# Kernel tuning notes

Hardware: AMD Instinct MI355X
Metric: run time of the kernel (lower is better)

The kernel has to match this reference:

```python
import jax, jax.numpy as jnp
import numpy as np

B, S, D, V = 2, 2048, 1024, 50257
GAMMA = 1.0
IGNORE = -100


def setup_inputs() -> dict:
    key = jax.random.key(0)
    k1, k2, k3, k4 = jax.random.split(key, 4)
    embeddings = jax.random.normal(k1, (B, S, D), dtype=jnp.float32)
    W = jax.random.normal(k2, (V, D), dtype=jnp.float32) * (D ** -0.5)
    b = jnp.zeros((V,), dtype=jnp.float32)
    labels = jax.random.randint(k3, (B, S), 0, V, dtype=jnp.int64)
    input_ids = jax.random.randint(k4, (B, S), 0, V, dtype=jnp.int64)
    return {"embeddings": embeddings, "W": W, "b": b, "labels": labels, "input_ids": input_ids}


def _focal_loss(embeddings, W, b, labels):
    # logits: [B, S, V]
    logits = jnp.einsum('bsd,vd->bsv', embeddings, W) + b
    shift_logits = logits[:, :-1, :].reshape(-1, V)          # [N, V]
    shift_labels = labels[:, 1:].reshape(-1)                  # [N]
    valid = shift_labels != IGNORE
    safe = jnp.where(valid, shift_labels, 0)
    logp = jax.nn.log_softmax(shift_logits, axis=-1)
    ce = -jnp.take_along_axis(logp, safe[:, None], axis=-1)[:, 0]
    ce = jnp.where(valid, ce, 0.0)                            # ignore_index -> 0 loss
    pt = jax.lax.stop_gradient(jnp.exp(-ce))
    w = (1.0 - pt) ** GAMMA
    alpha = 1.0 / jnp.mean(w)
    loss = alpha * w * ce
    return jnp.mean(loss)


def reference(embeddings, W, b, labels, input_ids):
    return _focal_loss(embeddings, W, b, labels)
```

## Files before the change

### kernel.cpp

```cpp
#include <hip/hip_runtime.h>
#include <hip/hip_bf16.h>
#include <cstdint>

#define SDIM   2048
#define DDIM   1024
#define VDIM   50257
#define VPAD   50304
#define NROWS  4094
#define MPAD   4096
#define NTM    32
#define NTN    393
#define NCHUNK (NTN * 2)
#define IGNORE_IDX (-100)

typedef __bf16 bf16x8 __attribute__((ext_vector_type(8)));
typedef float  f32x4  __attribute__((ext_vector_type(4)));

__device__ static inline unsigned short f2bf(float f) {
    union { float f; uint32_t u; } v; v.f = f;
    uint32_t u = v.u;
    return (unsigned short)((u + 0x7FFFu + ((u >> 16) & 1u)) >> 16);
}

__device__ static inline void gload_lds16(const void* g, void* l) {
    __builtin_amdgcn_global_load_lds(
        (const __attribute__((address_space(1))) unsigned int*)(g),
        (__attribute__((address_space(3))) unsigned int*)(l),
        16, 0, 0);
}

__global__ __launch_bounds__(256) void k_convert_W(const float* __restrict__ W,
                                                   unsigned short* __restrict__ Wb,
                                                   float* __restrict__ acc) {
    if (blockIdx.x == 0 && threadIdx.x < 2) acc[threadIdx.x] = 0.f;
    const int row = blockIdx.x;
    const int c4  = threadIdx.x << 2;
    ushort4 o;
    if (row < VDIM) {
        const float4 f = *(const float4*)(W + (size_t)row * DDIM + c4);
        o.x = f2bf(f.x); o.y = f2bf(f.y); o.z = f2bf(f.z); o.w = f2bf(f.w);
    } else {
        o.x = o.y = o.z = o.w = 0;
    }
    *(ushort4*)(Wb + (size_t)row * DDIM + c4) = o;
}

__global__ __launch_bounds__(256) void k_convert_A(const float* __restrict__ emb,
                                                   unsigned short* __restrict__ Ab) {
    const int row = blockIdx.x;
    const int c4  = threadIdx.x << 2;
    ushort4 o; o.x = o.y = o.z = o.w = 0;
    if (row < NROWS) {
        const int bb = row / 2047;
        const int s  = row - bb * 2047;
        const float4 f = *(const float4*)(emb + ((size_t)bb * SDIM + s) * DDIM + c4);
        o.x = f2bf(f.x); o.y = f2bf(f.y); o.z = f2bf(f.z); o.w = f2bf(f.w);
    }
    *(ushort4*)(Ab + (size_t)row * DDIM + c4) = o;
}

__global__ __launch_bounds__(256) void k_gemm(const unsigned short* __restrict__ Ab,
                                              const unsigned short* __restrict__ Wb,
                                              const float* __restrict__ bias,
                                              float2* __restrict__ Pml) {
    __shared__ unsigned short As[128 * 32];
    __shared__ unsigned short Bs[128 * 32];

    const int tid  = threadIdx.x;
    const int wave = tid >> 6, lane = tid & 63;
    const int q    = lane & 15, g = lane >> 4;
    const int wr   = wave >> 1, wc = wave & 1;
    const int bid  = blockIdx.x;
    const int tm   = bid & 31;
    const int tn   = bid >> 5;
    const size_t arow0 = (size_t)tm * 128;
    const size_t brow0 = (size_t)tn * 128;

    f32x4 acc[4][4];
    const f32x4 zf = {0.f, 0.f, 0.f, 0.f};
#pragma unroll
    for (int i = 0; i < 4; ++i)
#pragma unroll
        for (int j = 0; j < 4; ++j) acc[i][j] = zf;

#pragma unroll 1
    for (int kt = 0; kt < DDIM / 32; ++kt) {
        const int kbase = kt * 32;
#pragma unroll
        for (int j = 0; j < 2; ++j) {
            const int ci  = j * 256 + tid;
            const int row = ci >> 2;
            const int k8  = (ci & 3) * 8;
            gload_lds16(Ab + (arow0 + row) * DDIM + kbase + k8, &As[(j * 4 + wave) * 512]);
            gload_lds16(Wb + (brow0 + row) * DDIM + kbase + k8, &Bs[(j * 4 + wave) * 512]);
        }
        __syncthreads();
        bf16x8 af[4], bf[4];
#pragma unroll
        for (int mi = 0; mi < 4; ++mi)
            af[mi] = *(const bf16x8*)(As + (wr * 64 + mi * 16 + q) * 32 + g * 8);
#pragma unroll
        for (int ni = 0; ni < 4; ++ni)
            bf[ni] = *(const bf16x8*)(Bs + (wc * 64 + ni * 16 + q) * 32 + g * 8);
        __syncthreads();
#pragma unroll
        for (int mi = 0; mi < 4; ++mi)
#pragma unroll
            for (int ni = 0; ni < 4; ++ni)
                acc[mi][ni] = __builtin_amdgcn_mfma_f32_16x16x32_bf16(af[mi], bf[ni],
                                                                      acc[mi][ni], 0, 0, 0);
    }

    const float NEG_INF = -__builtin_inff();
    float bv[4]; int colv[4];
#pragma unroll
    for (int ni = 0; ni < 4; ++ni) {
        const int col = (int)brow0 + wc * 64 + ni * 16 + q;
        colv[ni] = col;
        bv[ni] = (col < VDIM) ? bias[col] : 0.f;
    }
#pragma unroll
    for (int mi = 0; mi < 4; ++mi) {
#pragma unroll
        for (int r = 0; r < 4; ++r) {
            float vv[4];
#pragma unroll
            for (int ni = 0; ni < 4; ++ni) {
                const float lv = acc[mi][ni][r] + bv[ni];
                vv[ni] = (colv[ni] < VDIM) ? lv : NEG_INF;
            }
            float m = fmaxf(fmaxf(vv[0], vv[1]), fmaxf(vv[2], vv[3]));
#pragma unroll
            for (int mask = 1; mask < 16; mask <<= 1) m = fmaxf(m, __shfl_xor(m, mask));
            float s = __expf(vv[0] - m) + __expf(vv[1] - m) +
                      __expf(vv[2] - m) + __expf(vv[3] - m);
#pragma unroll
            for (int mask = 1; mask < 16; mask <<= 1) s += __shfl_xor(s, mask);
            if (q == mi * 4 + r) {
                const int rowg = tm * 128 + wr * 64 + mi * 16 + g * 4 + r;
                Pml[(size_t)rowg * NCHUNK + (tn * 2 + wc)] = make_float2(m, s);
            }
        }
    }
}

__global__ __launch_bounds__(256) void k_finalize(const float2* __restrict__ Pml,
                                                  const float* __restrict__ emb,
                                                  const float* __restrict__ W,
                                                  const float* __restrict__ bias,
                                                  const int* __restrict__ labels,
                                                  float* __restrict__ acc) {
    const int r    = blockIdx.x;
    const int tid  = threadIdx.x;
    const int lane = tid & 63, wave = tid >> 6;
    const float NEG_INF = -__builtin_inff();

    float m = NEG_INF, l = 0.f;
    for (int c = tid; c < NCHUNK; c += 256) {
        const float2 p = Pml[(size_t)r * NCHUNK + c];
        const float mn = fmaxf(m, p.x);
        l = l * __expf(m - mn) + p.y * __expf(p.x - mn);
        m = mn;
    }
#pragma unroll
    for (int mask = 1; mask < 64; mask <<= 1) {
        const float om = __shfl_xor(m, mask);
        const float ol = __shfl_xor(l, mask);
        const float mn = fmaxf(m, om);
        l = l * __expf(m - mn) + ol * __expf(om - mn);
        m = mn;
    }

    const int bb = r / 2047;
    const int s  = r - bb * 2047;
    const int label = labels[bb * SDIM + s + 1];
    const bool valid = (label != IGNORE_IDX);
    const int lab = valid ? label : 0;
    const float* erow = emb + ((size_t)bb * SDIM + s) * DDIM;
    const float* wrow = W + (size_t)lab * DDIM;
    const float4 e  = *(const float4*)(erow + tid * 4);
    const float4 w4 = *(const float4*)(wrow + tid * 4);
    float d = e.x * w4.x + e.y * w4.y + e.z * w4.z + e.w * w4.w;
#pragma unroll
    for (int mask = 1; mask < 64; mask <<= 1) d += __shfl_xor(d, mask);

    __shared__ float sm[4], sl[4], sd[4];
    if (lane == 0) { sm[wave] = m; sl[wave] = l; sd[wave] = d; }
    __syncthreads();
    if (tid == 0) {
        float M = sm[0], L = sl[0];
#pragma unroll
        for (int wv = 1; wv < 4; ++wv) {
            const float mn = fmaxf(M, sm[wv]);
            L = L * __expf(M - mn) + sl[wv] * __expf(sm[wv] - mn);
            M = mn;
        }
        const float dot = sd[0] + sd[1] + sd[2] + sd[3];
        const float lse = M + logf(L);
        const float logit = dot + bias[lab];
        const float ce = valid ? (lse - logit) : 0.f;
        const float pt = __expf(-ce);
        const float w  = valid ? (1.f - pt) : 0.f;
        atomicAdd(acc + 0, w * ce);
        atomicAdd(acc + 1, w);
    }
}

__global__ void k_final(const float* __restrict__ acc, float* __restrict__ out) {
    out[0] = acc[0] / acc[1];
}

extern "C" void kernel_launch(void* const* d_in, const int* in_sizes, int n_in,
                              void* d_out, int out_size, void* d_ws, size_t ws_size,
                              hipStream_t stream) {
    const float* emb    = (const float*)d_in[0];
    const float* W      = (const float*)d_in[1];
    const float* bias   = (const float*)d_in[2];
    const int*   labels = (const int*)d_in[3];

    char* ws = (char*)d_ws;
    const size_t WB = (size_t)VPAD * DDIM * 2;
    const size_t AB = (size_t)MPAD * DDIM * 2;
    const size_t PB = (size_t)MPAD * NCHUNK * 8;
    unsigned short* Wb  = (unsigned short*)ws;
    unsigned short* Ab  = (unsigned short*)(ws + WB);
    float2*         Pml = (float2*)(ws + WB + AB);
    float*          acc = (float*)(ws + WB + AB + PB);

    k_convert_W<<<VPAD, 256, 0, stream>>>(W, Wb, acc);
    k_convert_A<<<MPAD, 256, 0, stream>>>(emb, Ab);
    k_gemm<<<NTM * NTN, 256, 0, stream>>>(Ab, Wb, bias, Pml);
    k_finalize<<<NROWS, 256, 0, stream>>>(Pml, emb, W, bias, labels, acc);
    k_final<<<1, 1, 0, stream>>>(acc, (float*)d_out);
}
```

Before: 1.005 ms.

## Rework GEMM to 256x256 tiles with double-buffered swizzled LDS pipeline

```diff
diff --git a/kernel.cpp b/kernel.cpp
--- a/kernel.cpp
+++ b/kernel.cpp
@@ -5,13 +5,15 @@
 #define SDIM   2048
 #define DDIM   1024
 #define VDIM   50257
-#define VPAD   50304
+#define VPAD   50432
 #define NROWS  4094
 #define MPAD   4096
-#define NTM    32
-#define NTN    393
-#define NCHUNK (NTN * 2)
+#define NTM    16
+#define NTN    197
+#define NCHUNK (NTN * 4)
+#define NKT    16
 #define IGNORE_IDX (-100)
+#define NEGBIG (-3.0e38f)
 
 typedef __bf16 bf16x8 __attribute__((ext_vector_type(8)));
 typedef float  f32x4  __attribute__((ext_vector_type(4)));
@@ -59,75 +61,121 @@
     *(ushort4*)(Ab + (size_t)row * DDIM + c4) = o;
 }
 
-__global__ __launch_bounds__(256) void k_gemm(const unsigned short* __restrict__ Ab,
-                                              const unsigned short* __restrict__ Wb,
-                                              const float* __restrict__ bias,
-                                              float2* __restrict__ Pml) {
-    __shared__ unsigned short As[128 * 32];
-    __shared__ unsigned short Bs[128 * 32];
+__global__ __launch_bounds__(512, 2) void k_gemm(const unsigned short* __restrict__ Ab,
+                                                 const unsigned short* __restrict__ Wb,
+                                                 const float* __restrict__ bias,
+                                                 float2* __restrict__ Pml) {
+    extern __shared__ unsigned short lds[];
+    unsigned short* As = lds;
+    unsigned short* Bs = lds + 2 * 256 * 64;
 
     const int tid  = threadIdx.x;
     const int wave = tid >> 6, lane = tid & 63;
     const int q    = lane & 15, g = lane >> 4;
-    const int wr   = wave >> 1, wc = wave & 1;
-    const int bid  = blockIdx.x;
-    const int tm   = bid & 31;
-    const int tn   = bid >> 5;
-    const size_t arow0 = (size_t)tm * 128;
-    const size_t brow0 = (size_t)tn * 128;
-
-    f32x4 acc[4][4];
+    const int wr   = wave >> 2;
+    const int wc   = wave & 3;
+
+    const int bid0 = (int)blockIdx.x;
+    const int bid  = (bid0 & 7) * (NTM * NTN / 8) + (bid0 >> 3);
+    const int tm   = bid & 15;
+    const int tn   = bid >> 4;
+    const size_t arow0 = (size_t)tm * 256;
+    const size_t brow0 = (size_t)tn * 256;
+
+    f32x4 acc[8][4];
     const f32x4 zf = {0.f, 0.f, 0.f, 0.f};
 #pragma unroll
-    for (int i = 0; i < 4; ++i)
+    for (int i = 0; i < 8; ++i)
 #pragma unroll
         for (int j = 0; j < 4; ++j) acc[i][j] = zf;
 
+    auto stage_unit = [&](const unsigned short* G, size_t grow0, int kt, int h,
+                          unsigned short* L) {
+#pragma unroll
+        for (int j = 0; j < 2; ++j) {
+            const int ci   = j * 512 + tid;
+            const int row  = h * 128 + (ci >> 3);
+            const int slot = ci & 7;
+            const int ss   = slot ^ (row & 7);
+            gload_lds16(G + (grow0 + row) * DDIM + kt * 64 + ss * 8,
+                        L + h * (128 * 64) + (size_t)(j * 512 + wave * 64) * 8);
+        }
+    };
+
+    auto phase = [&](int c, int mh, int ks, bool stA, bool stB, int ktn, bool do_vm) {
+        const unsigned short* Ac = As + c * (256 * 64);
+        const unsigned short* Bc = Bs + c * (256 * 64);
+        bf16x8 af[4], bfr[4];
+#pragma unroll
+        for (int fi = 0; fi < 4; ++fi) {
+            const int row = wr * 128 + mh * 64 + fi * 16 + q;
+            const int sl  = (ks * 4 + g) ^ (row & 7);
+            af[fi] = *(const bf16x8*)(Ac + row * 64 + sl * 8);
+        }
+#pragma unroll
+        for (int fj = 0; fj < 4; ++fj) {
+            const int row = wc * 64 + fj * 16 + q;
+            const int sl  = (ks * 4 + g) ^ (row & 7);
+            bfr[fj] = *(const bf16x8*)(Bc + row * 64 + sl * 8);
+        }
+        if (stA) {
+            stage_unit(Ab, arow0, ktn, 0, As + (c ^ 1) * (256 * 64));
+            stage_unit(Ab, arow0, ktn, 1, As + (c ^ 1) * (256 * 64));
+        }
+        if (stB) {
+            stage_unit(Wb, brow0, ktn, 0, Bs + (c ^ 1) * (256 * 64));
+            stage_unit(Wb, brow0, ktn, 1, Bs + (c ^ 1) * (256 * 64));
+        }
+        if (do_vm) asm volatile("s_waitcnt vmcnt(0)" ::: "memory");
+        __builtin_amdgcn_sched_barrier(0);
+        __builtin_amdgcn_s_barrier();
+        asm volatile("s_waitcnt lgkmcnt(0)" ::: "memory");
+        __builtin_amdgcn_sched_barrier(0);
+        __builtin_amdgcn_s_setprio(1);
+#pragma unroll
+        for (int fi = 0; fi < 4; ++fi)
+#pragma unroll
+            for (int fj = 0; fj < 4; ++fj)
+                acc[mh * 4 + fi][fj] = __builtin_amdgcn_mfma_f32_16x16x32_bf16(
+                    af[fi], bfr[fj], acc[mh * 4 + fi][fj], 0, 0, 0);
+        __builtin_amdgcn_s_setprio(0);
+        __builtin_amdgcn_sched_barrier(0);
+    };
+
+    stage_unit(Ab, arow0, 0, 0, As);
+    stage_unit(Ab, arow0, 0, 1, As);
+    stage_unit(Wb, brow0, 0, 0, Bs);
+    stage_unit(Wb, brow0, 0, 1, Bs);
+    asm volatile("s_waitcnt vmcnt(0)" ::: "memory");
+    __builtin_amdgcn_sched_barrier(0);
+    __builtin_amdgcn_s_barrier();
+
 #pragma unroll 1
-    for (int kt = 0; kt < DDIM / 32; ++kt) {
-        const int kbase = kt * 32;
-#pragma unroll
-        for (int j = 0; j < 2; ++j) {
-            const int ci  = j * 256 + tid;
-            const int row = ci >> 2;
-            const int k8  = (ci & 3) * 8;
-            gload_lds16(Ab + (arow0 + row) * DDIM + kbase + k8, &As[(j * 4 + wave) * 512]);
-            gload_lds16(Wb + (brow0 + row) * DDIM + kbase + k8, &Bs[(j * 4 + wave) * 512]);
-        }
-        __syncthreads();
-        bf16x8 af[4], bf[4];
-#pragma unroll
-        for (int mi = 0; mi < 4; ++mi)
-            af[mi] = *(const bf16x8*)(As + (wr * 64 + mi * 16 + q) * 32 + g * 8);
-#pragma unroll
-        for (int ni = 0; ni < 4; ++ni)
-            bf[ni] = *(const bf16x8*)(Bs + (wc * 64 + ni * 16 + q) * 32 + g * 8);
-        __syncthreads();
-#pragma unroll
-        for (int mi = 0; mi < 4; ++mi)
-#pragma unroll
-            for (int ni = 0; ni < 4; ++ni)
-                acc[mi][ni] = __builtin_amdgcn_mfma_f32_16x16x32_bf16(af[mi], bf[ni],
-                                                                      acc[mi][ni], 0, 0, 0);
-    }
-
-    const float NEG_INF = -__builtin_inff();
+    for (int t = 0; t < NKT; ++t) {
+        const int  c  = t & 1;
+        const bool st = (t < NKT - 1);
+        phase(c, 0, 0, st, false, t + 1, false);
+        phase(c, 0, 1, false, st, t + 1, false);
+        phase(c, 1, 0, false, false, t + 1, false);
+        phase(c, 1, 1, false, false, t + 1, true);
+    }
+
     float bv[4]; int colv[4];
 #pragma unroll
-    for (int ni = 0; ni < 4; ++ni) {
-        const int col = (int)brow0 + wc * 64 + ni * 16 + q;
-        colv[ni] = col;
-        bv[ni] = (col < VDIM) ? bias[col] : 0.f;
-    }
-#pragma unroll
-    for (int mi = 0; mi < 4; ++mi) {
+    for (int fj = 0; fj < 4; ++fj) {
+        const int col = tn * 256 + wc * 64 + fj * 16 + q;
+        colv[fj] = col;
+        bv[fj] = (col < VDIM) ? bias[col] : 0.f;
+    }
+#pragma unroll
+    for (int mf = 0; mf < 8; ++mf) {
 #pragma unroll
         for (int r = 0; r < 4; ++r) {
             float vv[4];
 #pragma unroll
-            for (int ni = 0; ni < 4; ++ni) {
-                const float lv = acc[mi][ni][r] + bv[ni];
-                vv[ni] = (colv[ni] < VDIM) ? lv : NEG_INF;
+            for (int fj = 0; fj < 4; ++fj) {
+                const float lv = acc[mf][fj][r] + bv[fj];
+                vv[fj] = (colv[fj] < VDIM) ? lv : NEGBIG;
             }
             float m = fmaxf(fmaxf(vv[0], vv[1]), fmaxf(vv[2], vv[3]));
 #pragma unroll
@@ -136,9 +184,9 @@
                       __expf(vv[2] - m) + __expf(vv[3] - m);
 #pragma unroll
             for (int mask = 1; mask < 16; mask <<= 1) s += __shfl_xor(s, mask);
-            if (q == mi * 4 + r) {
-                const int rowg = tm * 128 + wr * 64 + mi * 16 + g * 4 + r;
-                Pml[(size_t)rowg * NCHUNK + (tn * 2 + wc)] = make_float2(m, s);
+            if (q == ((mf * 4 + r) & 15)) {
+                const int rowg = tm * 256 + wr * 128 + mf * 16 + g * 4 + r;
+                Pml[(size_t)rowg * NCHUNK + (tn * 4 + wc)] = make_float2(m, s);
             }
         }
     }
@@ -153,9 +201,8 @@
     const int r    = blockIdx.x;
     const int tid  = threadIdx.x;
     const int lane = tid & 63, wave = tid >> 6;
-    const float NEG_INF = -__builtin_inff();
-
-    float m = NEG_INF, l = 0.f;
+
+    float m = NEGBIG, l = 0.f;
     for (int c = tid; c < NCHUNK; c += 256) {
         const float2 p = Pml[(size_t)r * NCHUNK + c];
         const float mn = fmaxf(m, p.x);
@@ -229,7 +276,7 @@
 
     k_convert_W<<<VPAD, 256, 0, stream>>>(W, Wb, acc);
     k_convert_A<<<MPAD, 256, 0, stream>>>(emb, Ab);
-    k_gemm<<<NTM * NTN, 256, 0, stream>>>(Ab, Wb, bias, Pml);
+    k_gemm<<<NTM * NTN, 512, 131072, stream>>>(Ab, Wb, bias, Pml);
     k_finalize<<<NROWS, 256, 0, stream>>>(Pml, emb, W, bias, labels, acc);
     k_final<<<1, 1, 0, stream>>>(acc, (float*)d_out);
 }
```

Result: faster. 909.8 us (-9.5%).
